# Performance work log

Measured on AMD Instinct MI355X. Metric: run time of the kernel, lower is better.

The kernel has to match this reference:

```python
import math
import jax, jax.numpy as jnp
import numpy as np


def _conv2d_same(x, w):
    # x: [B,C,H,W], w: [O,I,3,3] -> [B,O,H,W], stride 1, padding 1 (SAME)
    return jax.lax.conv_general_dilated(
        x, w, window_strides=(1, 1), padding='SAME',
        dimension_numbers=('NCHW', 'OIHW', 'NCHW'))


def setup_inputs() -> dict:
    key = jax.random.key(0)
    ks = jax.random.split(key, 7)
    B, CK, CV, T, H, W = 2, 64, 512, 8, 48, 48
    mk = jax.random.normal(ks[0], (B, CK, T, H, W), dtype=jnp.float32)
    qk = jax.random.normal(ks[1], (B, CK, H, W), dtype=jnp.float32)
    mv = jax.random.normal(ks[2], (B, CV, T, H, W), dtype=jnp.float32)
    qv = jax.random.normal(ks[3], (B, CV, H, W), dtype=jnp.float32)
    mask = jax.random.uniform(ks[4], (B, 1, H, W), dtype=jnp.float32)
    conv_w = jax.random.normal(ks[5], (1, 2 * CV + 1, 3, 3), dtype=jnp.float32) * 0.02
    conv_b = jnp.zeros((1,), dtype=jnp.float32)
    return {"mk": mk, "qk": qk, "mv": mv, "qv": qv, "mask": mask,
            "conv_w": conv_w, "conv_b": conv_b}


def reference(mk, qk, mv, qv, mask, conv_w, conv_b):
    B, CK, T, H, W = mk.shape
    CV = mv.shape[1]
    M, N = T * H * W, H * W  # memory tokens, query tokens

    # --- MemoryReader.get_affinity: L2-expanded attention over memory axis ---
    mkf = mk.reshape(B, CK, M)           # [B,CK,M]
    qkf = qk.reshape(B, CK, N)           # [B,CK,N]
    a_sq = jnp.sum(mkf * mkf, axis=1)[:, :, None]            # [B,M,1]
    ab = jnp.einsum('bcm,bcn->bmn', mkf, qkf)                # [B,M,N]
    affinity = (2.0 * ab - a_sq) / math.sqrt(CK)
    affinity = jax.nn.softmax(affinity, axis=1)              # softmax over memory tokens

    # --- MemoryReader.readout: bmm readout + concat with query value ---
    mo = mv.reshape(B, CV, M)                                # [B,CV,M]
    mem = jnp.einsum('bcm,bmn->bcn', mo, affinity).reshape(B, CV, H, W)
    mem_out = jnp.concatenate([mem, qv], axis=1)             # [B,2*CV,H,W]

    # --- STCN.segment gating chain: conv(cat(mem, mask)) -> sigmoid -> gate ---
    gate_in = jnp.concatenate([mem_out, mask], axis=1)       # [B,2*CV+1,H,W]
    gate = jax.nn.sigmoid(_conv2d_same(gate_in, conv_w) + conv_b[None, :, None, None])
    return mem_out * gate
```

## Files before the change

kernel.cpp:

```cpp
#include <hip/hip_runtime.h>

#define B_  2
#define CK_ 64
#define CV_ 512
#define H_  48
#define W_  48
#define M_  18432
#define N_  2304

#define SSPLIT 8
#define MSEG   (M_ / SSPLIT)
#define VSTRIDE16 (CV_ * 16)

typedef __bf16 bf16x8 __attribute__((ext_vector_type(8)));
typedef float  f32x4  __attribute__((ext_vector_type(4)));
typedef float  f32x16 __attribute__((ext_vector_type(16)));
typedef unsigned int u32x4 __attribute__((ext_vector_type(4)));

#define C2Q   0.36067376f
#define C_KSQ 0.18033688f

__device__ inline f32x16 mfma32(bf16x8 a, bf16x8 b, f32x16 c) {
    return __builtin_amdgcn_mfma_f32_32x32x16_bf16(a, b, c, 0, 0, 0);
}

__device__ inline unsigned pack_bf16(float lo, float hi) {
    union { __bf16 h; unsigned short u; } a, b;
    a.h = (__bf16)lo; b.h = (__bf16)hi;
    return ((unsigned)b.u << 16) | a.u;
}

__device__ __forceinline__ void gload_lds16(const __bf16* g, __bf16* l) {
    __builtin_amdgcn_global_load_lds(
        (const __attribute__((address_space(1))) void*)g,
        (__attribute__((address_space(3))) void*)l,
        16, 0, 0);
}

__global__ __launch_bounds__(256) void prep_k(const float* __restrict__ mk,
                                              __bf16* __restrict__ ktile,
                                              unsigned* __restrict__ ksq2) {
    const int idx = blockIdx.x * 256 + threadIdx.x;
    const int b = idx / M_, m = idx % M_;
    const float* src = mk + (size_t)b * CK_ * M_ + m;
    const int mt = m >> 5, l = m & 31;
    __bf16* dstb = ktile + (size_t)b * M_ * 64 + (size_t)mt * 2048 + l * 8;
    float s = 0.f;
#pragma unroll
    for (int j = 0; j < 8; ++j) {
        bf16x8 o;
#pragma unroll
        for (int i = 0; i < 8; ++i) {
            float v = src[(size_t)(8 * j + i) * M_];
            s += v * v;
            o[i] = (__bf16)v;
        }
        *(bf16x8*)(dstb + (size_t)j * 256) = o;
    }
    const float tot = s * C_KSQ;
    const float hi = (float)(__bf16)tot;
    const float lo = tot - hi;
    ksq2[idx] = pack_bf16(hi, lo);
}

__global__ __launch_bounds__(256) void prep_v(const float* __restrict__ mv,
                                              __bf16* __restrict__ vt) {
    const int idx = blockIdx.x * 256 + threadIdx.x;
    const int c   = idx % CV_;
    const int r   = idx / CV_;
    const int m16 = r % (M_ / 16);
    const int b   = r / (M_ / 16);
    const float4* s4 = (const float4*)(mv + ((size_t)b * CV_ + c) * M_ + m16 * 16);
    const float4 a0 = s4[0], a1 = s4[1], a2 = s4[2], a3 = s4[3];
    bf16x8 o0, o1;
    o0[0]=(__bf16)a0.x; o0[1]=(__bf16)a0.y; o0[2]=(__bf16)a0.z; o0[3]=(__bf16)a0.w;
    o0[4]=(__bf16)a1.x; o0[5]=(__bf16)a1.y; o0[6]=(__bf16)a1.z; o0[7]=(__bf16)a1.w;
    o1[0]=(__bf16)a2.x; o1[1]=(__bf16)a2.y; o1[2]=(__bf16)a2.z; o1[3]=(__bf16)a2.w;
    o1[4]=(__bf16)a3.x; o1[5]=(__bf16)a3.y; o1[6]=(__bf16)a3.z; o1[7]=(__bf16)a3.w;
    __bf16* dst = vt + ((size_t)r * CV_ + c) * 16;
    *(bf16x8*)dst = o0;
    *(bf16x8*)(dst + 8) = o1;
}


#define LOADK(k0, k1, k2, k3, kq) do {                                        \
    k0 = *(const bf16x8*)(kp + koff);                                         \
    k1 = *(const bf16x8*)(kp + koff + 512);                                   \
    k2 = *(const bf16x8*)(kp + koff + 1024);                                  \
    k3 = *(const bf16x8*)(kp + koff + 1536);                                  \
    kq = kqp[l31];                                                            \
    kp += 2048; kqp += 32;                                                    \
} while (0)

#define STAGEV(vnxt) do {                                                     \
    _Pragma("unroll")                                                         \
    for (int i = 0; i < 4; ++i) {                                             \
        const int j = i * 4 + w;                                              \
        const int chunk = j >> 3, off = j & 7;                                \
        gload_lds16(vps + chunk * VSTRIDE16 + cwoff + off * 512 + soff,       \
                    (vnxt) + chunk * 4096 + off * 512);                       \
    }                                                                         \
    vps += 2 * VSTRIDE16;                                                     \
} while (0)

#define BODY(vcur, vnxt, STAGE, RELOADK) do {                                 \
    __syncthreads();                                                          \
    if (STAGE) STAGEV(vnxt);                                                  \
    u32x4 _a4u = { h ? 0u : kqC, 0u, 0u, 0u };                                \
    const bf16x8 _af4 = __builtin_bit_cast(bf16x8, _a4u);                     \
    __builtin_amdgcn_s_setprio(1);                                            \
    f32x16 _d = mfma32(_af4, bneg, fzero);                                    \
    _d = mfma32(kC0, qf[0], _d);                                              \
    _d = mfma32(kC1, qf[1], _d);                                              \
    _d = mfma32(kC2, qf[2], _d);                                              \
    _d = mfma32(kC3, qf[3], _d);                                              \
    __builtin_amdgcn_s_setprio(0);                                            \
    if (RELOADK) LOADK(kC0, kC1, kC2, kC3, kqC);       \
    unsigned _wpk[8];                                                         \
    _Pragma("unroll")                                                         \
    for (int j = 0; j < 8; ++j) {                                             \
        const float _pa = __builtin_amdgcn_exp2f(_d[2*j]);                    \
        const float _pc = __builtin_amdgcn_exp2f(_d[2*j+1]);                  \
        den[j & 3] += _pa + _pc;                                              \
        _wpk[j] = pack_bf16(_pa, _pc);                                        \
    }                                                                         \
    bf16x8 _pb0, _pb1;                                                        \
    {                                                                         \
        unsigned _a0 = _wpk[0], _b0 = _wpk[2];                                \
        unsigned _a1 = _wpk[1], _b1 = _wpk[3];                                \
        asm volatile("v_permlane32_swap_b32 %0, %1" : "+v"(_a0), "+v"(_b0));  \
        asm volatile("v_permlane32_swap_b32 %0, %1" : "+v"(_a1), "+v"(_b1));  \
        u32x4 _pu = {_a0, _a1, _b0, _b1};                                     \
        _pb0 = __builtin_bit_cast(bf16x8, _pu);                               \
    }                                                                         \
    {                                                                         \
        unsigned _a0 = _wpk[4], _b0 = _wpk[6];                                \
        unsigned _a1 = _wpk[5], _b1 = _wpk[7];                                \
        asm volatile("v_permlane32_swap_b32 %0, %1" : "+v"(_a0), "+v"(_b0));  \
        asm volatile("v_permlane32_swap_b32 %0, %1" : "+v"(_a1), "+v"(_b1));  \
        u32x4 _pu = {_a0, _a1, _b0, _b1};                                     \
        _pb1 = __builtin_bit_cast(bf16x8, _pu);                               \
    }                                                                         \
                  \
    _Pragma("unroll")                                                         \
    for (int j = 0; j < 4; ++j)                                               \
        va[j] = *(const bf16x8*)((vcur) + j * 512 + vloff);                   \
    _Pragma("unroll")                                                         \
    for (int j = 0; j < 4; ++j)                                               \
        vb[j] = *(const bf16x8*)((vcur) + (4 + j) * 512 + vloff);             \
    __builtin_amdgcn_s_setprio(1);                                            \
    _Pragma("unroll")                                                         \
    for (int j = 0; j < 4; ++j)                                               \
        acc[j] = mfma32(va[j], _pb0, acc[j]);                                 \
    __builtin_amdgcn_s_setprio(0);                                            \
    _Pragma("unroll")                                                         \
    for (int j = 0; j < 4; ++j)                                               \
        va[j] = *(const bf16x8*)((vcur) + 4096 + j * 512 + vloff);            \
    __builtin_amdgcn_s_setprio(1);                                            \
    _Pragma("unroll")                                                         \
    for (int j = 0; j < 4; ++j)                                               \
        acc[4 + j] = mfma32(vb[j], _pb0, acc[4 + j]);                         \
    __builtin_amdgcn_s_setprio(0);                                            \
    _Pragma("unroll")                                                         \
    for (int j = 0; j < 4; ++j)                                               \
        vb[j] = *(const bf16x8*)((vcur) + 4096 + (4 + j) * 512 + vloff);      \
    __builtin_amdgcn_s_setprio(1);                                            \
    _Pragma("unroll")                                                         \
    for (int j = 0; j < 4; ++j)                                               \
        acc[j] = mfma32(va[j], _pb1, acc[j]);                                 \
    _Pragma("unroll")                                                         \
    for (int j = 0; j < 4; ++j)                                               \
        acc[4 + j] = mfma32(vb[j], _pb1, acc[4 + j]);                         \
    __builtin_amdgcn_s_setprio(0);                                            \
} while (0)

__global__ __launch_bounds__(256, 2) void flash12_kernel(const __bf16* __restrict__ ktile,
                                                         const float* __restrict__ qk,
                                                         const __bf16* __restrict__ vt,
                                                         const unsigned* __restrict__ ksq2,
                                                         __bf16* __restrict__ partO,
                                                         float* __restrict__ partD) {
    const int tid = threadIdx.x;
    const int w = tid >> 6, lane = tid & 63;
    const int l31 = lane & 31, h = lane >> 5;

    const int bid = blockIdx.x;
    const int xcd = bid & 7;
    const int ixc = bid >> 3;
    const int grp = ixc / 18;
    const int blk = ixc % 18;
    const int G   = xcd * 4 + grp;
    const int cs2 = G & 1;
    const int sb  = G >> 1;
    const int s   = sb & 7, b = sb >> 3;
    const int nt  = blk * 4 + w;

    const int n0 = nt * 32;
    const int cw = cs2 * 256;
    const int m_base = s * MSEG;

    const int koff  = (h * 32 + l31) * 8;
    const int vloff = lane * 8;
    const int cwoff = cw * 16;
    const int soff  = (lane & 31) * 16 + (lane >> 5) * 8;

    __shared__ __align__(16) __bf16 Vlds[2][8192];

    const float* qkb = qk + (size_t)b * CK_ * N_;
    bf16x8 qf[4];
#pragma unroll
    for (int ks = 0; ks < 4; ++ks)
#pragma unroll
      for (int i = 0; i < 8; ++i)
        qf[ks][i] = (__bf16)(qkb[(size_t)(16*ks + 8*h + i) * N_ + (n0 + l31)] * C2Q);

    const u32x4 bneg_u = {0xBF80BF80u, 0u, 0u, 0u};
    const bf16x8 bneg = __builtin_bit_cast(bf16x8, bneg_u);

    f32x16 fzero;
#pragma unroll
    for (int r = 0; r < 16; ++r) fzero[r] = 0.f;

    const __bf16*   kp  = ktile + (size_t)b * M_ * 64 + (size_t)m_base * 64;
    const unsigned* kqp = ksq2  + (size_t)b * M_ + m_base;
    const __bf16*   vps = vt    + (size_t)b * M_ * CV_ + (size_t)m_base * CV_;

    f32x16 acc[8];
#pragma unroll
    for (int ct = 0; ct < 8; ++ct)
#pragma unroll
      for (int r = 0; r < 16; ++r) acc[ct][r] = 0.f;
    float den[4] = {0.f, 0.f, 0.f, 0.f};

    bf16x8 kC0, kC1, kC2, kC3;
    unsigned kqC;
    bf16x8 va[4], vb[4];

    LOADK(kC0, kC1, kC2, kC3, kqC);
    STAGEV(&Vlds[0][0]);

    for (int mss = 0; mss < 35; ++mss) {
        BODY(&Vlds[0][0], &Vlds[1][0], 1, 1);
        BODY(&Vlds[1][0], &Vlds[0][0], 1, 1);
    }
    BODY(&Vlds[0][0], &Vlds[1][0], 1, 1);
    BODY(&Vlds[1][0], &Vlds[0][0], 0, 0);

    float dsum = (den[0] + den[1]) + (den[2] + den[3]);
    dsum += __shfl_xor(dsum, 32);
    if (cs2 == 0 && lane < 32)
        partD[(size_t)(s * B_ + b) * N_ + n0 + l31] = dsum;

    __bf16* po = partO + (((size_t)(s * B_ + b) * CV_ + cw) * N_) + n0 + l31;
#pragma unroll
    for (int ct = 0; ct < 8; ++ct)
#pragma unroll
      for (int r = 0; r < 16; ++r) {
        const int crow = 32*ct + (r & 3) + 8*(r >> 2) + 4*h;
        po[(size_t)crow * N_] = (__bf16)acc[ct][r];
      }
}

__global__ __launch_bounds__(256) void reduce_kernel(const __bf16* __restrict__ partO,
                                                     const float* __restrict__ partD,
                                                     float* __restrict__ out) {
    const int idx = blockIdx.x * 256 + threadIdx.x;
    const int n8 = idx % (N_ / 8);
    const int c  = (idx / (N_ / 8)) % CV_;
    const int b  = idx / ((N_ / 8) * CV_);
    float o[8] = {0,0,0,0,0,0,0,0};
    float dd[8] = {0,0,0,0,0,0,0,0};
#pragma unroll
    for (int s = 0; s < SSPLIT; ++s) {
        const bf16x8 ov = *(const bf16x8*)(partO + (((size_t)(s*B_+b)*CV_ + c) * N_) + n8*8);
        const float4 d0 = *(const float4*)(partD + (size_t)(s*B_+b)*N_ + n8*8);
        const float4 d1 = *(const float4*)(partD + (size_t)(s*B_+b)*N_ + n8*8 + 4);
#pragma unroll
        for (int j = 0; j < 8; ++j) o[j] += (float)ov[j];
        dd[0]+=d0.x; dd[1]+=d0.y; dd[2]+=d0.z; dd[3]+=d0.w;
        dd[4]+=d1.x; dd[5]+=d1.y; dd[6]+=d1.z; dd[7]+=d1.w;
    }
    float* op = out + ((size_t)b * (2*CV_) + c) * N_ + n8*8;
#pragma unroll
    for (int j = 0; j < 8; ++j) op[j] = o[j] / dd[j];
}

__global__ __launch_bounds__(256) void conv_r_kernel(const float* __restrict__ outf,
                                                     const float* __restrict__ qv,
                                                     const float* __restrict__ mask,
                                                     const float* __restrict__ cw,
                                                     float* __restrict__ Rp) {
    const int p  = blockIdx.x * 256 + threadIdx.x;
    const int cc = blockIdx.y;
    const int b  = blockIdx.z;
    float r[9] = {0,0,0,0,0,0,0,0,0};
    if (cc < 8) {
        const float* src = (cc < 4) ? outf + ((size_t)b * (2*CV_) + cc * 128) * N_
                                    : qv   + ((size_t)b * CV_ + (cc - 4) * 128) * N_;
        const float* wb = cw + (size_t)cc * 128 * 9;
        for (int c = 0; c < 128; ++c) {
            const float v = src[(size_t)c * N_ + p];
#pragma unroll
            for (int j = 0; j < 9; ++j) r[j] += v * wb[c * 9 + j];
        }
    } else {
        const float v = mask[(size_t)b * N_ + p];
#pragma unroll
        for (int j = 0; j < 9; ++j) r[j] = v * cw[1024 * 9 + j];
    }
#pragma unroll
    for (int j = 0; j < 9; ++j)
        Rp[(((size_t)cc * 9 + j) * B_ + b) * N_ + p] = r[j];
}

__global__ __launch_bounds__(256) void gate_kernel(const float* __restrict__ Rp,
                                                   const float* __restrict__ cbias,
                                                   float* __restrict__ gate_ws) {
    const int p = blockIdx.x * 256 + threadIdx.x;
    const int b = blockIdx.y;
    const int y = p / W_, x = p % W_;
    float sum = cbias[0];
#pragma unroll
    for (int dy = -1; dy <= 1; ++dy) {
        const int yy = y + dy;
        if (yy < 0 || yy >= H_) continue;
#pragma unroll
        for (int dx = -1; dx <= 1; ++dx) {
            const int xx = x + dx;
            if (xx < 0 || xx >= W_) continue;
            const int j = (dy + 1) * 3 + (dx + 1);
            const int q = yy * W_ + xx;
#pragma unroll
            for (int cc = 0; cc < 9; ++cc)
                sum += Rp[(((size_t)cc * 9 + j) * B_ + b) * N_ + q];
        }
    }
    gate_ws[(size_t)b * N_ + p] = 1.f / (1.f + __builtin_amdgcn_exp2f(-sum * 1.44269504f));
}

__global__ __launch_bounds__(256) void finalize_kernel(const float* __restrict__ qv,
                                                       const float* __restrict__ gate_ws,
                                                       float* __restrict__ out) {
    const int idx = blockIdx.x * 256 + threadIdx.x;
    const int n4 = N_ / 4;
    const int pos4 = idx % n4;
    const int row  = idx / n4;
    const int b = row >> 10, ch = row & 1023;
    const float4 gv = *(const float4*)(gate_ws + (size_t)b * N_ + pos4 * 4);
    float* op = out + (size_t)row * N_ + pos4 * 4;
    float4 v;
    if (ch < CV_) v = *(const float4*)op;
    else          v = *(const float4*)(qv + ((size_t)b * CV_ + (ch - CV_)) * N_ + pos4 * 4);
    v.x *= gv.x; v.y *= gv.y; v.z *= gv.z; v.w *= gv.w;
    *(float4*)op = v;
}

extern "C" void kernel_launch(void* const* d_in, const int* in_sizes, int n_in,
                              void* d_out, int out_size, void* d_ws, size_t ws_size,
                              hipStream_t stream) {
    (void)in_sizes; (void)n_in; (void)out_size; (void)ws_size;
    const float* mk    = (const float*)d_in[0];
    const float* qk    = (const float*)d_in[1];
    const float* mv    = (const float*)d_in[2];
    const float* qv    = (const float*)d_in[3];
    const float* mask  = (const float*)d_in[4];
    const float* cw    = (const float*)d_in[5];
    const float* cbias = (const float*)d_in[6];
    float* outf = (float*)d_out;

    const size_t kbf_b   = (size_t)B_ * M_ * 64 * 2;
    const size_t vbf_b   = (size_t)B_ * CV_ * M_ * 2;
    const size_t ksq_b   = (size_t)B_ * M_ * 4;
    const size_t partO_b = (size_t)SSPLIT * B_ * CV_ * N_ * 2;
    const size_t partD_b = (size_t)SSPLIT * B_ * N_ * 4;

    char* pw = (char*)d_ws;
    __bf16* ktile = (__bf16*)pw;
    float*  Rp    = (float*)pw;
    pw += kbf_b;
    __bf16* vt    = (__bf16*)pw;           pw += vbf_b;
    unsigned* ksq2 = (unsigned*)pw;        pw += ksq_b;
    __bf16* partO = (__bf16*)pw;           pw += partO_b;
    float*  partD = (float*)pw;            pw += partD_b;
    float*  gate_ws = (float*)pw;

    prep_k<<<dim3(B_ * M_ / 256), 256, 0, stream>>>(mk, ktile, ksq2);
    prep_v<<<dim3((size_t)B_ * (M_ / 16) * CV_ / 256, 1, 1), 256, 0, stream>>>(mv, vt);
    flash12_kernel<<<dim3(576), 256, 0, stream>>>(ktile, qk, vt, ksq2, partO, partD);
    reduce_kernel<<<dim3(B_ * CV_ * (N_ / 8) / 256), 256, 0, stream>>>(partO, partD, outf);
    conv_r_kernel<<<dim3(N_ / 256, 9, B_), 256, 0, stream>>>(outf, qv, mask, cw, Rp);
    gate_kernel<<<dim3(N_ / 256, B_), 256, 0, stream>>>(Rp, cbias, gate_ws);
    finalize_kernel<<<dim3((B_ * 2 * CV_ * N_ / 4) / 256), 256, 0, stream>>>(qv, gate_ws, outf);
}
```

Before: 232.7 us.

## Share one QK/softmax tile per block, rotating duty across waves via LDS

Before, each of the four waves in a block handled its own 32-query tile and its own 256-channel half, so every wave recomputed QK scores and exp. Now all four waves in a block share a single 32-query tile and split the 512 output channels 128 each. The waves take turns computing the score and exp tile one step ahead and publish the bf16 probabilities through a double-buffered LDS buffer, with K loads prefetched several steps ahead. This removes redundant QK MFMAs and exponentials and halves the accumulator registers per wave, at the cost of twice as many blocks, larger V staging in LDS, an extra LDS round trip for P, and an LDS reduction of the denominator.

```diff
diff --git a/kernel.cpp b/kernel.cpp
--- a/kernel.cpp
+++ b/kernel.cpp
@@ -83,29 +83,18 @@
 }
 
 
-#define LOADK(k0, k1, k2, k3, kq) do {                                        \
-    k0 = *(const bf16x8*)(kp + koff);                                         \
-    k1 = *(const bf16x8*)(kp + koff + 512);                                   \
-    k2 = *(const bf16x8*)(kp + koff + 1024);                                  \
-    k3 = *(const bf16x8*)(kp + koff + 1536);                                  \
-    kq = kqp[l31];                                                            \
-    kp += 2048; kqp += 32;                                                    \
-} while (0)
-
 #define STAGEV(vnxt) do {                                                     \
     _Pragma("unroll")                                                         \
-    for (int i = 0; i < 4; ++i) {                                             \
+    for (int i = 0; i < 8; ++i) {                                             \
         const int j = i * 4 + w;                                              \
-        const int chunk = j >> 3, off = j & 7;                                \
-        gload_lds16(vps + chunk * VSTRIDE16 + cwoff + off * 512 + soff,       \
-                    (vnxt) + chunk * 4096 + off * 512);                       \
+        const int chunk = j >> 4, off = j & 15;                               \
+        gload_lds16(vps + chunk * VSTRIDE16 + off * 512 + soff,               \
+                    (vnxt) + chunk * 8192 + off * 512);                       \
     }                                                                         \
     vps += 2 * VSTRIDE16;                                                     \
 } while (0)
 
-#define BODY(vcur, vnxt, STAGE, RELOADK) do {                                 \
-    __syncthreads();                                                          \
-    if (STAGE) STAGEV(vnxt);                                                  \
+#define DUTY(pdst) do {                                                       \
     u32x4 _a4u = { h ? 0u : kqC, 0u, 0u, 0u };                                \
     const bf16x8 _af4 = __builtin_bit_cast(bf16x8, _a4u);                     \
     __builtin_amdgcn_s_setprio(1);                                            \
@@ -115,7 +104,6 @@
     _d = mfma32(kC2, qf[2], _d);                                              \
     _d = mfma32(kC3, qf[3], _d);                                              \
     __builtin_amdgcn_s_setprio(0);                                            \
-    if (RELOADK) LOADK(kC0, kC1, kC2, kC3, kqC);       \
     unsigned _wpk[8];                                                         \
     _Pragma("unroll")                                                         \
     for (int j = 0; j < 8; ++j) {                                             \
@@ -124,14 +112,14 @@
         den[j & 3] += _pa + _pc;                                              \
         _wpk[j] = pack_bf16(_pa, _pc);                                        \
     }                                                                         \
-    bf16x8 _pb0, _pb1;                                                        \
+    bf16x8 _pb0h, _pb1h;                                                      \
     {                                                                         \
         unsigned _a0 = _wpk[0], _b0 = _wpk[2];                                \
         unsigned _a1 = _wpk[1], _b1 = _wpk[3];                                \
         asm volatile("v_permlane32_swap_b32 %0, %1" : "+v"(_a0), "+v"(_b0));  \
         asm volatile("v_permlane32_swap_b32 %0, %1" : "+v"(_a1), "+v"(_b1));  \
         u32x4 _pu = {_a0, _a1, _b0, _b1};                                     \
-        _pb0 = __builtin_bit_cast(bf16x8, _pu);                               \
+        _pb0h = __builtin_bit_cast(bf16x8, _pu);                              \
     }                                                                         \
     {                                                                         \
         unsigned _a0 = _wpk[4], _b0 = _wpk[6];                                \
@@ -139,42 +127,52 @@
         asm volatile("v_permlane32_swap_b32 %0, %1" : "+v"(_a0), "+v"(_b0));  \
         asm volatile("v_permlane32_swap_b32 %0, %1" : "+v"(_a1), "+v"(_b1));  \
         u32x4 _pu = {_a0, _a1, _b0, _b1};                                     \
-        _pb1 = __builtin_bit_cast(bf16x8, _pu);                               \
+        _pb1h = __builtin_bit_cast(bf16x8, _pu);                              \
     }                                                                         \
-                  \
-    _Pragma("unroll")                                                         \
-    for (int j = 0; j < 4; ++j)                                               \
-        va[j] = *(const bf16x8*)((vcur) + j * 512 + vloff);                   \
-    _Pragma("unroll")                                                         \
-    for (int j = 0; j < 4; ++j)                                               \
-        vb[j] = *(const bf16x8*)((vcur) + (4 + j) * 512 + vloff);             \
+    *(bf16x8*)((pdst) + lane * 8)       = _pb0h;                              \
+    *(bf16x8*)((pdst) + 512 + lane * 8) = _pb1h;                              \
+} while (0)
+
+#define LOADK_AT(t) do {                                                      \
+    const __bf16* _kpt = kp + (size_t)(t) * 2048;                             \
+    kC0 = *(const bf16x8*)(_kpt + koff);                                      \
+    kC1 = *(const bf16x8*)(_kpt + koff + 512);                                \
+    kC2 = *(const bf16x8*)(_kpt + koff + 1024);                               \
+    kC3 = *(const bf16x8*)(_kpt + koff + 1536);                               \
+    kqC = kqp[(t) * 32 + l31];                                                \
+} while (0)
+
+#define BODY(vcur, vnxt, pcur, pnxt, STAGE, DOQK) do {                        \
+    __syncthreads();                                                          \
+    if (STAGE) STAGEV(vnxt);                                                  \
+    if (DOQK && w == ((scur + 1) & 3)) {                                      \
+        DUTY(pnxt);                                                           \
+        if (scur <= 66) LOADK_AT(scur + 5);                                   \
+    }                                                                         \
+    const bf16x8 _pb0 = *(const bf16x8*)((pcur) + vloff);                     \
+    const bf16x8 _pb1 = *(const bf16x8*)((pcur) + 512 + vloff);               \
+    const bf16x8 _va0 = *(const bf16x8*)((vcur) + w2048 + vloff);             \
+    const bf16x8 _va1 = *(const bf16x8*)((vcur) + w2048 + 512 + vloff);       \
+    const bf16x8 _va2 = *(const bf16x8*)((vcur) + w2048 + 1024 + vloff);      \
+    const bf16x8 _va3 = *(const bf16x8*)((vcur) + w2048 + 1536 + vloff);      \
+    const bf16x8 _vb0 = *(const bf16x8*)((vcur) + 8192 + w2048 + vloff);      \
+    const bf16x8 _vb1 = *(const bf16x8*)((vcur) + 8192 + w2048 + 512 + vloff);\
+    const bf16x8 _vb2 = *(const bf16x8*)((vcur) + 8192 + w2048 + 1024 + vloff);\
+    const bf16x8 _vb3 = *(const bf16x8*)((vcur) + 8192 + w2048 + 1536 + vloff);\
     __builtin_amdgcn_s_setprio(1);                                            \
-    _Pragma("unroll")                                                         \
-    for (int j = 0; j < 4; ++j)                                               \
-        acc[j] = mfma32(va[j], _pb0, acc[j]);                                 \
+    acc[0] = mfma32(_va0, _pb0, acc[0]);                                      \
+    acc[1] = mfma32(_va1, _pb0, acc[1]);                                      \
+    acc[2] = mfma32(_va2, _pb0, acc[2]);                                      \
+    acc[3] = mfma32(_va3, _pb0, acc[3]);                                      \
+    acc[0] = mfma32(_vb0, _pb1, acc[0]);                                      \
+    acc[1] = mfma32(_vb1, _pb1, acc[1]);                                      \
+    acc[2] = mfma32(_vb2, _pb1, acc[2]);                                      \
+    acc[3] = mfma32(_vb3, _pb1, acc[3]);                                      \
     __builtin_amdgcn_s_setprio(0);                                            \
-    _Pragma("unroll")                                                         \
-    for (int j = 0; j < 4; ++j)                                               \
-        va[j] = *(const bf16x8*)((vcur) + 4096 + j * 512 + vloff);            \
-    __builtin_amdgcn_s_setprio(1);                                            \
-    _Pragma("unroll")                                                         \
-    for (int j = 0; j < 4; ++j)                                               \
-        acc[4 + j] = mfma32(vb[j], _pb0, acc[4 + j]);                         \
-    __builtin_amdgcn_s_setprio(0);                                            \
-    _Pragma("unroll")                                                         \
-    for (int j = 0; j < 4; ++j)                                               \
-        vb[j] = *(const bf16x8*)((vcur) + 4096 + (4 + j) * 512 + vloff);      \
-    __builtin_amdgcn_s_setprio(1);                                            \
-    _Pragma("unroll")                                                         \
-    for (int j = 0; j < 4; ++j)                                               \
-        acc[j] = mfma32(va[j], _pb1, acc[j]);                                 \
-    _Pragma("unroll")                                                         \
-    for (int j = 0; j < 4; ++j)                                               \
-        acc[4 + j] = mfma32(vb[j], _pb1, acc[4 + j]);                         \
-    __builtin_amdgcn_s_setprio(0);                                            \
+    ++scur;                                                                   \
 } while (0)
 
-__global__ __launch_bounds__(256, 2) void flash12_kernel(const __bf16* __restrict__ ktile,
+__global__ __launch_bounds__(256, 2) void flash13_kernel(const __bf16* __restrict__ ktile,
                                                          const float* __restrict__ qk,
                                                          const __bf16* __restrict__ vt,
                                                          const unsigned* __restrict__ ksq2,
@@ -187,24 +185,22 @@
     const int bid = blockIdx.x;
     const int xcd = bid & 7;
     const int ixc = bid >> 3;
-    const int grp = ixc / 18;
-    const int blk = ixc % 18;
-    const int G   = xcd * 4 + grp;
-    const int cs2 = G & 1;
-    const int sb  = G >> 1;
-    const int s   = sb & 7, b = sb >> 3;
-    const int nt  = blk * 4 + w;
+    const int grp = ixc / 72;
+    const int nt  = ixc % 72;
+    const int G   = xcd * 2 + grp;
+    const int s   = G & 7, b = G >> 3;
 
     const int n0 = nt * 32;
-    const int cw = cs2 * 256;
     const int m_base = s * MSEG;
 
     const int koff  = (h * 32 + l31) * 8;
     const int vloff = lane * 8;
-    const int cwoff = cw * 16;
     const int soff  = (lane & 31) * 16 + (lane >> 5) * 8;
-
-    __shared__ __align__(16) __bf16 Vlds[2][8192];
+    const int w2048 = w * 2048;
+
+    __shared__ __align__(16) __bf16 Vlds[2][16384];
+    __shared__ __align__(16) __bf16 Plds[2][1024];
+    __shared__ float dred[4][32];
 
     const float* qkb = qk + (size_t)b * CK_ * N_;
     bf16x8 qf[4];
@@ -225,35 +221,47 @@
     const unsigned* kqp = ksq2  + (size_t)b * M_ + m_base;
     const __bf16*   vps = vt    + (size_t)b * M_ * CV_ + (size_t)m_base * CV_;
 
-    f32x16 acc[8];
-#pragma unroll
-    for (int ct = 0; ct < 8; ++ct)
+    f32x16 acc[4];
+#pragma unroll
+    for (int ct = 0; ct < 4; ++ct)
 #pragma unroll
       for (int r = 0; r < 16; ++r) acc[ct][r] = 0.f;
     float den[4] = {0.f, 0.f, 0.f, 0.f};
 
     bf16x8 kC0, kC1, kC2, kC3;
     unsigned kqC;
-    bf16x8 va[4], vb[4];
-
-    LOADK(kC0, kC1, kC2, kC3, kqC);
+    int scur = 0;
+
     STAGEV(&Vlds[0][0]);
-
-    for (int mss = 0; mss < 35; ++mss) {
-        BODY(&Vlds[0][0], &Vlds[1][0], 1, 1);
-        BODY(&Vlds[1][0], &Vlds[0][0], 1, 1);
-    }
-    BODY(&Vlds[0][0], &Vlds[1][0], 1, 1);
-    BODY(&Vlds[1][0], &Vlds[0][0], 0, 0);
+    {
+        const int t0 = (w == 0) ? 0 : w;
+        LOADK_AT(t0);
+    }
+    if (w == 0) {
+        DUTY(&Plds[0][0]);
+        LOADK_AT(4);
+    }
+
+    for (int it = 0; it < 35; ++it) {
+        BODY(&Vlds[0][0], &Vlds[1][0], &Plds[0][0], &Plds[1][0], 1, 1);
+        BODY(&Vlds[1][0], &Vlds[0][0], &Plds[1][0], &Plds[0][0], 1, 1);
+    }
+    BODY(&Vlds[0][0], &Vlds[1][0], &Plds[0][0], &Plds[1][0], 1, 1);
+    BODY(&Vlds[1][0], &Vlds[0][0], &Plds[1][0], &Plds[0][0], 0, 0);
 
     float dsum = (den[0] + den[1]) + (den[2] + den[3]);
     dsum += __shfl_xor(dsum, 32);
-    if (cs2 == 0 && lane < 32)
-        partD[(size_t)(s * B_ + b) * N_ + n0 + l31] = dsum;
-
-    __bf16* po = partO + (((size_t)(s * B_ + b) * CV_ + cw) * N_) + n0 + l31;
-#pragma unroll
-    for (int ct = 0; ct < 8; ++ct)
+    __syncthreads();
+    if (lane < 32) dred[w][l31] = dsum;
+    __syncthreads();
+    if (tid < 32) {
+        const float tot = (dred[0][tid] + dred[1][tid]) + (dred[2][tid] + dred[3][tid]);
+        partD[(size_t)(s * B_ + b) * N_ + n0 + tid] = tot;
+    }
+
+    __bf16* po = partO + (((size_t)(s * B_ + b) * CV_ + 128 * w) * N_) + n0 + l31;
+#pragma unroll
+    for (int ct = 0; ct < 4; ++ct)
 #pragma unroll
       for (int r = 0; r < 16; ++r) {
         const int crow = 32*ct + (r & 3) + 8*(r >> 2) + 4*h;
@@ -386,7 +394,7 @@
 
     prep_k<<<dim3(B_ * M_ / 256), 256, 0, stream>>>(mk, ktile, ksq2);
     prep_v<<<dim3((size_t)B_ * (M_ / 16) * CV_ / 256, 1, 1), 256, 0, stream>>>(mv, vt);
-    flash12_kernel<<<dim3(576), 256, 0, stream>>>(ktile, qk, vt, ksq2, partO, partD);
+    flash13_kernel<<<dim3(1152), 256, 0, stream>>>(ktile, qk, vt, ksq2, partO, partD);
     reduce_kernel<<<dim3(B_ * CV_ * (N_ / 8) / 256), 256, 0, stream>>>(partO, partD, outf);
     conv_r_kernel<<<dim3(N_ / 256, 9, B_), 256, 0, stream>>>(outf, qv, mask, cw, Rp);
     gate_kernel<<<dim3(N_ / 256, B_), 256, 0, stream>>>(Rp, cbias, gate_ws);
```

Result: slower. 301.3 us (+29.5%).
